# Kernel tuning notes

Hardware: AMD Instinct MI355X
Metric: run time of the kernel (lower is better)

The kernel has to match this reference:

```python
import jax, jax.numpy as jnp
import numpy as np

W_DIM = 512
FREQ = 1024
CH = 512
OUT_CH = 512
SIZE = 64
SR = 64.0
BW = 2.0
MAX_BW = BW * 8.0
B = 16
K = 3


def setup_inputs() -> dict:
    key = jax.random.key(0)
    ks = jax.random.split(key, 10)
    w = jax.random.normal(ks[0], (B, W_DIM), dtype=jnp.float32)
    # SynthesisInput buffers: random unit-direction freqs scaled by uniform radius in [0, max_bw)
    f = jax.random.normal(ks[1], (FREQ, 2), dtype=jnp.float32)
    f = f / jnp.linalg.norm(f, axis=1, keepdims=True)
    freqs = f * (jax.random.uniform(ks[2], (FREQ, 1), dtype=jnp.float32) * MAX_BW)
    phases = jax.random.uniform(ks[3], (FREQ,), dtype=jnp.float32) - 0.5
    input_weight = jax.random.normal(ks[4], (CH, FREQ), dtype=jnp.float32)
    # affine: FullyConnectedLayer(w_dim, 4, weight_init=0, bias_init=[1,0,0,0])
    affine_w = jnp.zeros((4, W_DIM), dtype=jnp.float32)
    affine_b = jnp.array([1.0, 0.0, 0.0, 0.0], dtype=jnp.float32)
    # per-layer style affine (w -> in_channels), bias_init=1 (StyleGAN convention)
    style_w = jax.random.normal(ks[5], (CH, W_DIM), dtype=jnp.float32)
    style_b = jnp.ones((CH,), dtype=jnp.float32)
    conv_w = jax.random.normal(ks[6], (OUT_CH, CH, K, K), dtype=jnp.float32)
    conv_b = jnp.zeros((OUT_CH,), dtype=jnp.float32)
    return {"w": w, "affine_w": affine_w, "affine_b": affine_b, "freqs": freqs,
            "phases": phases, "input_weight": input_weight, "style_w": style_w,
            "style_b": style_b, "conv_w": conv_w, "conv_b": conv_b}


def _fc(x, weight, bias):
    # FullyConnectedLayer: weight_gain = 1/sqrt(in_features)
    gain = 1.0 / np.sqrt(weight.shape[1])
    return x @ (weight * gain).T + bias


def _synthesis_input(w, affine_w, affine_b, freqs, phases, input_weight):
    t = _fc(w, affine_w, affine_b)                                  # [B,4]
    t = t / jnp.linalg.norm(t[:, :2], axis=1, keepdims=True)
    c, s, tx, ty = t[:, 0], t[:, 1], t[:, 2], t[:, 3]
    # m = m_r @ m_t (only the 2x3 top block matters)
    rot = jnp.stack([jnp.stack([c, -s], -1), jnp.stack([s, c], -1)], 1)  # [B,2,2]
    trans = jnp.stack([-tx, -ty], -1)                               # [B,2]
    shift = jnp.einsum('bij,bj->bi', rot, trans)                    # [B,2]
    phases_b = phases[None, :] + jnp.einsum('fi,bi->bf', freqs, shift)
    freqs_b = jnp.einsum('fi,bij->bfj', freqs, rot)                 # [B,F,2]
    amp = jnp.clip(1.0 - (jnp.linalg.norm(freqs_b, axis=2) - BW) / (SR / 2.0 - BW), 0.0, 1.0)
    # affine_grid(theta=diag(0.5*size/sr)=0.5, align_corners=False)
    theta00 = 0.5 * SIZE / SR
    xs = ((jnp.arange(SIZE, dtype=jnp.float32) + 0.5) / SIZE * 2.0 - 1.0) * theta00
    ys = ((jnp.arange(SIZE, dtype=jnp.float32) + 0.5) / SIZE * 2.0 - 1.0) * theta00
    gx, gy = jnp.meshgrid(xs, ys)                                   # [H,W]
    grid = jnp.stack([gx, gy], axis=-1)                             # [H,W,2]
    x = jnp.einsum('hwi,bfi->bhwf', grid, freqs_b) + phases_b[:, None, None, :]
    x = jnp.sin(x * (2.0 * np.pi)) * amp[:, None, None, :]
    effect_freq = jnp.sum((jnp.linalg.norm(freqs, axis=-1) < BW).astype(jnp.float32))
    x = jnp.einsum('bhwf,cf->bchw', x, input_weight / jnp.sqrt(effect_freq))
    return x                                                        # [B,CH,H,W]


def _modulated_conv2d(x, weight, s, padding=1):
    # demodulate: pre-normalize w and s
    w_hat = weight * jax.lax.rsqrt(jnp.mean(jnp.square(weight), axis=(1, 2, 3), keepdims=True))
    s_hat = s * jax.lax.rsqrt(jnp.mean(jnp.square(s)))
    # dcoefs[b,o] = rsqrt(sum_ikl (w[o,i,k,l]*s[b,i])^2 + eps)
    dcoefs = jax.lax.rsqrt(jnp.einsum('oikl,bi->bo', jnp.square(w_hat), jnp.square(s_hat)) + 1e-8)
    # grouped-per-sample conv == scale input channels by s, conv with base w, scale out by dcoefs
    x = x * s_hat[:, :, None, None]
    y = jax.lax.conv_general_dilated(x, w_hat, window_strides=(1, 1),
                                     padding=[(padding, padding), (padding, padding)],
                                     dimension_numbers=('NCHW', 'OIHW', 'NCHW'))
    return y * dcoefs[:, :, None, None]


def reference(w, affine_w, affine_b, freqs, phases, input_weight, style_w, style_b, conv_w, conv_b):
    x = _synthesis_input(w, affine_w, affine_b, freqs, phases, input_weight)
    s = _fc(w, style_w, style_b)                                    # [B,CH]
    y = _modulated_conv2d(x, conv_w, s, padding=K // 2)
    y = y + conv_b[None, :, None, None]
    y = jnp.where(y >= 0, y, 0.2 * y) * np.sqrt(2.0)                # lrelu + gain (bias_act)
    y = jnp.clip(y, -256.0, 256.0)                                  # conv_clamp
    return y
```

## Files before the change

### kernel.cpp

```cpp
#include <hip/hip_runtime.h>

typedef __attribute__((ext_vector_type(4))) float f32x4;
typedef __attribute__((ext_vector_type(8))) __bf16 bf16x8;

__device__ __forceinline__ unsigned short f2bf(float f) {
  unsigned int u = __builtin_bit_cast(unsigned int, f);
  return (unsigned short)((u + 0x7FFFu + ((u >> 16) & 1u)) >> 16);
}

__device__ __forceinline__ float sin2pi(float x) {
#if __has_builtin(__builtin_amdgcn_sinf) && __has_builtin(__builtin_amdgcn_fractf)
  return __builtin_amdgcn_sinf(__builtin_amdgcn_fractf(x));
#else
  return __sinf(x * 6.283185307179586f);
#endif
}

__device__ __forceinline__ void gll16(const void* g, void* l) {
  __builtin_amdgcn_global_load_lds(
      (const __attribute__((address_space(1))) void*)g,
      (__attribute__((address_space(3))) void*)l, 16, 0, 0);
}

template <int W>
__device__ __forceinline__ void vmwait() {
  if constexpr (W == 0) asm volatile("s_waitcnt vmcnt(0)" ::: "memory");
  else if constexpr (W == 2) asm volatile("s_waitcnt vmcnt(2)" ::: "memory");
  else if constexpr (W == 4) asm volatile("s_waitcnt vmcnt(4)" ::: "memory");
  else if constexpr (W == 6) asm volatile("s_waitcnt vmcnt(6)" ::: "memory");
  else if constexpr (W == 8) asm volatile("s_waitcnt vmcnt(8)" ::: "memory");
}

#define CFENCE() asm volatile("" ::: "memory")

__global__ void prep_freq_k(const float* __restrict__ w, const float* __restrict__ affine_w,
                            const float* __restrict__ affine_b, const float* __restrict__ freqs,
                            const float* __restrict__ phases, float4* __restrict__ freq_data,
                            float* __restrict__ scal) {
  const int b = blockIdx.x, tid = threadIdx.x;
  const int wv = tid >> 6, lane = tid & 63;
  __shared__ float tdot[4];
  __shared__ float par[4];
  __shared__ float scnt;
  float sum = 0.f;
  for (int i = lane; i < 512; i += 64) sum += w[b * 512 + i] * affine_w[wv * 512 + i];
#pragma unroll
  for (int o = 32; o > 0; o >>= 1) sum += __shfl_down(sum, o);
  if (lane == 0) tdot[wv] = sum;
  if (tid == 0) scnt = 0.f;
  __syncthreads();
  if (tid == 0) {
    const float gain = 0.04419417382415922f;
    float t0 = tdot[0] * gain + affine_b[0];
    float t1 = tdot[1] * gain + affine_b[1];
    float t2 = tdot[2] * gain + affine_b[2];
    float t3 = tdot[3] * gain + affine_b[3];
    float inv = 1.f / sqrtf(t0 * t0 + t1 * t1);
    float c = t0 * inv, s = t1 * inv, tx = t2 * inv, ty = t3 * inv;
    par[0] = c; par[1] = s;
    par[2] = -c * tx + s * ty;
    par[3] = -s * tx - c * ty;
  }
  __syncthreads();
  const float c = par[0], s = par[1], sh0 = par[2], sh1 = par[3];
  float cnt = 0.f;
  for (int f = tid; f < 1024; f += 256) {
    float fx = freqs[2 * f], fy = freqs[2 * f + 1];
    float fb0 = fx * c + fy * s;
    float fb1 = fy * c - fx * s;
    float ph = phases[f] + fx * sh0 + fy * sh1;
    float nb = sqrtf(fb0 * fb0 + fb1 * fb1);
    float amp = fminf(fmaxf(1.f - (nb - 2.f) * (1.f / 30.f), 0.f), 1.f);
    float4 v; v.x = fb0; v.y = fb1; v.z = ph; v.w = amp;
    freq_data[(b << 10) + f] = v;
    if (sqrtf(fx * fx + fy * fy) < 2.f) cnt += 1.f;
  }
  if (b == 0) {
    atomicAdd(&scnt, cnt);
    __syncthreads();
    if (tid == 0) scal[0] = 1.f / sqrtf(scnt);
  }
}

__global__ void style_k(const float* __restrict__ w, const float* __restrict__ style_w,
                        const float* __restrict__ style_b, float* __restrict__ s_out) {
  int idx = blockIdx.x * 256 + threadIdx.x;
  int b = idx >> 9, c = idx & 511;
  const float gain = 0.04419417382415922f;
  const float4* wr = (const float4*)(w + b * 512);
  const float4* sr = (const float4*)(style_w + (size_t)c * 512);
  float sum = 0.f;
#pragma unroll 4
  for (int i = 0; i < 128; ++i) {
    float4 a = wr[i], q = sr[i];
    sum += a.x * q.x + a.y * q.y + a.z * q.z + a.w * q.w;
  }
  s_out[idx] = sum * gain + style_b[c];
}

__global__ void convw_prep_k(const float* __restrict__ conv_w, float* __restrict__ wsumT,
                             unsigned short* __restrict__ bt_conv) {
  const int o = blockIdx.x, tid = threadIdx.x;
  __shared__ float red[256];
  float sum = 0.f;
  for (int i = tid; i < 4608; i += 256) { float v = conv_w[o * 4608 + i]; sum += v * v; }
  red[tid] = sum;
  __syncthreads();
  for (int off = 128; off > 0; off >>= 1) {
    if (tid < off) red[tid] += red[tid + off];
    __syncthreads();
  }
  const float rn = rsqrtf(red[0] * (1.f / 4608.f));
  for (int i = tid; i < 512; i += 256) {
    float sq = 0.f;
#pragma unroll
    for (int kl = 0; kl < 9; ++kl) {
      float v = conv_w[(o * 512 + i) * 9 + kl];
      sq += v * v;
      bt_conv[o * 4608 + kl * 512 + i] = f2bf(v * rn);
    }
    wsumT[i * 512 + o] = sq * rn * rn;
  }
}

__global__ void iw_cast_k(const float* __restrict__ iw, unsigned short* __restrict__ iw_bf) {
  int i = blockIdx.x * 256 + threadIdx.x;
  iw_bf[i] = f2bf(iw[i]);
}

__global__ void shat_dcoef_k(const float* __restrict__ s, const float* __restrict__ wsumT,
                             float* __restrict__ s_hat, float* __restrict__ dcoefs) {
  const int b = blockIdx.x, tid = threadIdx.x;
  __shared__ float red[256];
  __shared__ float sh2[512];
  float sum = 0.f;
  for (int i = tid; i < 8192; i += 256) { float v = s[i]; sum += v * v; }
  red[tid] = sum;
  __syncthreads();
  for (int off = 128; off > 0; off >>= 1) {
    if (tid < off) red[tid] += red[tid + off];
    __syncthreads();
  }
  const float inv_rms = rsqrtf(red[0] * (1.f / 8192.f));
  for (int c = tid; c < 512; c += 256) {
    float sh = s[b * 512 + c] * inv_rms;
    s_hat[b * 512 + c] = sh;
    sh2[c] = sh * sh;
  }
  __syncthreads();
  for (int o = tid; o < 512; o += 256) {
    float acc = 0.f;
    for (int i = 0; i < 512; ++i) acc += wsumT[i * 512 + o] * sh2[i];
    dcoefs[b * 512 + o] = rsqrtf(acc + 1e-8f);
  }
}

__global__ void border_zero_k(unsigned short* __restrict__ xmp) {
  int idx = blockIdx.x * 256 + threadIdx.x;
  int chunk = idx & 63;
  int t = idx >> 6;
  int p = t % 260;
  int b = t / 260;
  int h, w;
  if (p < 66) { h = 0; w = p; }
  else if (p < 132) { h = 65; w = p - 66; }
  else if (p < 196) { h = p - 131; w = 0; }
  else { h = p - 195; w = 65; }
  uint4 z; z.x = 0; z.y = 0; z.z = 0; z.w = 0;
  *(uint4*)&xmp[(((size_t)b * 66 + h) * 66 + w) * 512 + chunk * 8] = z;
}

__device__ __forceinline__ void sy_sgB(char* lB, const unsigned short* iw, int n0, int d,
                                       int rb, int kt, int lane, int lsw) {
  const unsigned short* src = iw + (size_t)(n0 + rb + (lane >> 3)) * 1024 + (kt << 6) + lsw;
  gll16(src, lB + d * 32768 + rb * 128);
}

__global__ __launch_bounds__(256, 2) void synth_gemm2_k(
    const float4* __restrict__ freq_data, const unsigned short* __restrict__ iw_bf,
    const float* __restrict__ s_hat, const float* __restrict__ scal,
    unsigned short* __restrict__ xmp) {
  extern __shared__ char sl[];
  char* lA = sl;
  char* lB = sl + 16384;
  const int bid = blockIdx.x;
  const int mt = bid >> 1, nt = bid & 1;
  const int m0 = mt << 7, n0 = nt << 8;
  const int b = m0 >> 12;
  const int hbase = (m0 >> 6) & 63;
  const int tid = threadIdx.x, lane = tid & 63, wv = tid >> 6;
  const int wm = (wv >> 1) << 6, wn = (wv & 1) << 7;
  const int g = tid & 15;
  const int r0 = (tid >> 4) << 3;
  const int lsw = (((lane & 7) ^ (lane >> 3)) << 3);
  const int aswz = (((lane >> 4) << 4)) ^ ((lane & 7) << 4);
  const char* pA = lA + (size_t)(wm + (lane & 15)) * 128;
  const int browB = wn + (lane & 15);
  f32x4 acc[4][8];
#pragma unroll
  for (int mi = 0; mi < 4; ++mi)
#pragma unroll
    for (int ni = 0; ni < 8; ++ni) { f32x4 z = {0.f, 0.f, 0.f, 0.f}; acc[mi][ni] = z; }
  const float gy0 = (hbase + 0.5f) * 0.015625f - 0.5f;
  const float gy1 = (hbase + 1.5f) * 0.015625f - 0.5f;

#pragma unroll
  for (int ig = 0; ig < 8; ++ig) sy_sgB(lB, iw_bf, n0, 0, wv * 64 + ig * 8, 0, lane, lsw);
  vmwait<0>();
  __builtin_amdgcn_s_barrier();
  CFENCE();

  for (int kt = 0; kt < 16; ++kt) {
    if (kt < 15) {
#pragma unroll
      for (int ig = 0; ig < 8; ++ig)
        sy_sgB(lB, iw_bf, n0, (kt + 1) & 1, wv * 64 + ig * 8, kt + 1, lane, lsw);
    }
    const float4* fdp = freq_data + (b << 10) + (kt << 6) + (g << 2);
    float4 fd0 = fdp[0], fd1 = fdp[1], fd2 = fdp[2], fd3 = fdp[3];
#pragma unroll
    for (int j = 0; j < 8; ++j) {
      const int r = r0 + j;
      const float gx = ((r & 63) + 0.5f) * 0.015625f - 0.5f;
      const float gy = (r >> 6) ? gy1 : gy0;
      ushort4 u;
      u.x = f2bf(sin2pi(gx * fd0.x + gy * fd0.y + fd0.z) * fd0.w);
      u.y = f2bf(sin2pi(gx * fd1.x + gy * fd1.y + fd1.z) * fd1.w);
      u.z = f2bf(sin2pi(gx * fd2.x + gy * fd2.y + fd2.z) * fd2.w);
      u.w = f2bf(sin2pi(gx * fd3.x + gy * fd3.y + fd3.z) * fd3.w);
      *(ushort4*)(lA + r * 128 + ((g << 3) ^ (j << 4))) = u;
    }
    asm volatile("s_waitcnt lgkmcnt(0)" ::: "memory");
    if (kt < 15) vmwait<8>(); else vmwait<0>();
    __builtin_amdgcn_s_barrier();
    CFENCE();
    __builtin_amdgcn_sched_barrier(0);

    const char* pB = lB + ((kt & 1) << 15) + (size_t)browB * 128;
#pragma unroll
    for (int ks = 0; ks < 2; ++ks) {
      const int ao = aswz ^ (ks << 6);
      bf16x8 af[4], bq[8];
#pragma unroll
      for (int mi = 0; mi < 4; ++mi) af[mi] = *(const bf16x8*)(pA + mi * 2048 + ao);
#pragma unroll
      for (int ni = 0; ni < 8; ++ni) bq[ni] = *(const bf16x8*)(pB + ni * 2048 + ao);
      __builtin_amdgcn_s_setprio(1);
#pragma unroll
      for (int mi = 0; mi < 4; ++mi)
#pragma unroll
        for (int ni = 0; ni < 8; ++ni)
          acc[mi][ni] = __builtin_amdgcn_mfma_f32_16x16x32_bf16(af[mi], bq[ni], acc[mi][ni], 0, 0, 0);
      __builtin_amdgcn_s_setprio(0);
    }
    CFENCE();
    __builtin_amdgcn_s_barrier();
    CFENCE();
  }

  const float inv_eff = scal[0];
  const int c_lo = lane & 15, r_hi = (lane >> 4) << 2;
#pragma unroll
  for (int ni = 0; ni < 8; ++ni) {
    const int cc = n0 + wn + (ni << 4) + c_lo;
    const float sc = s_hat[b * 512 + cc] * inv_eff;
#pragma unroll
    for (int mi = 0; mi < 4; ++mi) {
#pragma unroll
      for (int j = 0; j < 4; ++j) {
        const int rr = wm + (mi << 4) + r_hi + j;
        const int hp = hbase + (rr >> 6) + 1;
        const int wp = (rr & 63) + 1;
        xmp[(((size_t)b * 66 + hp) * 66 + wp) * 512 + cc] = f2bf(acc[mi][ni][j] * sc);
      }
    }
  }
}

__device__ __forceinline__ float epi_act(float a, float dco, float cb) {
  float y = a * dco + cb;
  y = (y >= 0.f ? y : 0.2f * y) * 1.4142135623730951f;
  return fminf(fmaxf(y, -256.f), 256.f);
}

struct ConvCtx {
  const unsigned short* xmp;
  const unsigned short* bt;
  int n0, hb, b_img, lane;
  int lsw;
  int gB_rb0;
  int gA_lo;
  int gA_up;
};

__device__ __forceinline__ void tile_geom(int t, int& dh, int& dw, int& kc, int& koff) {
  const int kc8 = t / 9;
  const int off = t - 9 * kc8;
  dh = off / 3;
  dw = off - 3 * dh;
  kc = kc8 << 6;
  koff = off * 512 + kc;
}

__device__ __forceinline__ void sgA(char* lds, const ConvCtx& c, int d, int rb,
                                    int dh, int dw, int kc) {
  const int r = rb + (c.lane >> 3);
  const int h = c.hb + (r >> 6) + dh;
  const int w = (r & 63) + dw;
  const unsigned short* src = c.xmp + (((size_t)c.b_img * 66 + h) * 66 + w) * 512 + kc + c.lsw;
  gll16(src, lds + d * 32768 + rb * 128);
}

__device__ __forceinline__ void sgB(char* lds, const ConvCtx& c, int d, int rb, int koff) {
  const int row = c.n0 + rb + (c.lane >> 3);
  const unsigned short* src = c.bt + (size_t)row * 4608 + koff + c.lsw;
  gll16(src, lds + 65536 + d * 32768 + rb * 128);
}

#define PHASE_SYNC()                                        \
  __builtin_amdgcn_s_barrier();                             \
  asm volatile("s_waitcnt lgkmcnt(0)" ::: "memory");        \
  __builtin_amdgcn_sched_barrier(0);

#define PHASE_END()                                         \
  CFENCE();                                                 \
  __builtin_amdgcn_s_barrier();                             \
  CFENCE();

template <int D, int W0, bool SB, bool SAU, bool SAL>
__device__ __forceinline__ void conv_tile(char* lds, const ConvCtx& c, f32x4 (&acc)[8][4],
                                          const char* pA, const char* pB, int aswz0, int t) {
  int dh1, dw1, kc1, koff1, dh2, dw2, kc2, koff2;
  tile_geom(t + 1, dh1, dw1, kc1, koff1);
  tile_geom(t + 2, dh2, dw2, kc2, koff2);
  const int a0 = aswz0, a1 = aswz0 ^ 64;
  bf16x8 bq[4];
  {
#pragma unroll
    for (int ni = 0; ni < 4; ++ni) bq[ni] = *(const bf16x8*)(pB + D * 32768 + ni * 2048 + a0);
    bf16x8 af[4];
#pragma unroll
    for (int i = 0; i < 4; ++i) af[i] = *(const bf16x8*)(pA + D * 32768 + i * 2048 + a0);
    if (SB) { sgB(lds, c, D ^ 1, c.gB_rb0, koff1); sgB(lds, c, D ^ 1, c.gB_rb0 + 8, koff1); }
    if (W0 >= 0) vmwait<W0>();
    PHASE_SYNC();
    __builtin_amdgcn_s_setprio(1);
#pragma unroll
    for (int i = 0; i < 4; ++i)
#pragma unroll
      for (int ni = 0; ni < 4; ++ni)
        acc[i][ni] = __builtin_amdgcn_mfma_f32_16x16x32_bf16(af[i], bq[ni], acc[i][ni], 0, 0, 0);
    __builtin_amdgcn_s_setprio(0);
    PHASE_END();
  }
  {
    bf16x8 af[4];
#pragma unroll
    for (int i = 0; i < 4; ++i) af[i] = *(const bf16x8*)(pA + D * 32768 + (4 + i) * 2048 + a0);
    if (SB) { sgB(lds, c, D ^ 1, c.gB_rb0 + 16, koff1); sgB(lds, c, D ^ 1, c.gB_rb0 + 24, koff1); }
    PHASE_SYNC();
    __builtin_amdgcn_s_setprio(1);
#pragma unroll
    for (int i = 0; i < 4; ++i)
#pragma unroll
      for (int ni = 0; ni < 4; ++ni)
        acc[4 + i][ni] = __builtin_amdgcn_mfma_f32_16x16x32_bf16(af[i], bq[ni], acc[4 + i][ni], 0, 0, 0);
    __builtin_amdgcn_s_setprio(0);
    PHASE_END();
  }
  {
#pragma unroll
    for (int ni = 0; ni < 4; ++ni) bq[ni] = *(const bf16x8*)(pB + D * 32768 + ni * 2048 + a1);
    bf16x8 af[4];
#pragma unroll
    for (int i = 0; i < 4; ++i) af[i] = *(const bf16x8*)(pA + D * 32768 + i * 2048 + a1);
    if (SAU) { sgA(lds, c, D ^ 1, c.gA_up, dh1, dw1, kc1); sgA(lds, c, D ^ 1, c.gA_up + 8, dh1, dw1, kc1); }
    PHASE_SYNC();
    __builtin_amdgcn_s_setprio(1);
#pragma unroll
    for (int i = 0; i < 4; ++i)
#pragma unroll
      for (int ni = 0; ni < 4; ++ni)
        acc[i][ni] = __builtin_amdgcn_mfma_f32_16x16x32_bf16(af[i], bq[ni], acc[i][ni], 0, 0, 0);
    __builtin_amdgcn_s_setprio(0);
    PHASE_END();
  }
  {
    bf16x8 af[4];
#pragma unroll
    for (int i = 0; i < 4; ++i) af[i] = *(const bf16x8*)(pA + D * 32768 + (4 + i) * 2048 + a1);
    if (SAL) { sgA(lds, c, D, c.gA_lo, dh2, dw2, kc2); sgA(lds, c, D, c.gA_lo + 8, dh2, dw2, kc2); }
    PHASE_SYNC();
    __builtin_amdgcn_s_setprio(1);
#pragma unroll
    for (int i = 0; i < 4; ++i)
#pragma unroll
      for (int ni = 0; ni < 4; ++ni)
        acc[4 + i][ni] = __builtin_amdgcn_mfma_f32_16x16x32_bf16(af[i], bq[ni], acc[4 + i][ni], 0, 0, 0);
    __builtin_amdgcn_s_setprio(0);
    PHASE_END();
  }
}

__global__ __launch_bounds__(512, 2) void conv_gemm8_k(
    const unsigned short* __restrict__ xmp, const unsigned short* __restrict__ bt_conv,
    const float* __restrict__ dcoefs, const float* __restrict__ conv_b,
    float* __restrict__ out) {
  extern __shared__ char lds[];
  const int tid = threadIdx.x, lane = tid & 63, wv = tid >> 6;
  const int bid = blockIdx.x;
  const int wg = (bid & 7) * 64 + (bid >> 3);
  const int mt = wg >> 1, nt = wg & 1;
  const int m0 = mt << 8, n0 = nt << 8;
  const int b_img = m0 >> 12;
  const int hb = (m0 >> 6) & 63;
  const int wm = (wv >> 2) << 7, wn = (wv & 3) << 6;

  ConvCtx c;
  c.xmp = xmp; c.bt = bt_conv;
  c.n0 = n0; c.hb = hb; c.b_img = b_img; c.lane = lane;
  c.lsw = (((lane & 7) ^ (lane >> 3)) << 3);
  c.gB_rb0 = (((wv & 3) >> 1) << 7) + (((wv & 1) | ((wv >> 2) << 1)) << 5);
  c.gA_lo = wm + ((wv & 3) << 4);
  c.gA_up = c.gA_lo + 64;

  const char* pA = lds + (size_t)(wm + (lane & 15)) * 128;
  const char* pB = lds + 65536 + (size_t)(wn + (lane & 15)) * 128;
  const int aswz0 = (((lane >> 4) << 4)) ^ ((lane & 7) << 4);

  f32x4 acc[8][4];
#pragma unroll
  for (int mi = 0; mi < 8; ++mi)
#pragma unroll
    for (int ni = 0; ni < 4; ++ni) { f32x4 z = {0.f, 0.f, 0.f, 0.f}; acc[mi][ni] = z; }

  sgB(lds, c, 0, c.gB_rb0, 0);       sgB(lds, c, 0, c.gB_rb0 + 8, 0);
  sgB(lds, c, 0, c.gB_rb0 + 16, 0);  sgB(lds, c, 0, c.gB_rb0 + 24, 0);
  sgA(lds, c, 0, c.gA_up, 0, 0, 0);  sgA(lds, c, 0, c.gA_up + 8, 0, 0, 0);
  sgA(lds, c, 0, c.gA_lo, 0, 0, 0);  sgA(lds, c, 0, c.gA_lo + 8, 0, 0, 0);
  {
    int dh1, dw1, kc1, koff1;
    tile_geom(1, dh1, dw1, kc1, koff1);
    sgA(lds, c, 1, c.gA_lo, dh1, dw1, kc1);
    sgA(lds, c, 1, c.gA_lo + 8, dh1, dw1, kc1);
  }
  vmwait<2>();
  __builtin_amdgcn_s_barrier();
  CFENCE();

  for (int it = 0; it < 35; ++it) {
    conv_tile<0, 4, true, true, true>(lds, c, acc, pA, pB, aswz0, 2 * it);
    conv_tile<1, 4, true, true, true>(lds, c, acc, pA, pB, aswz0, 2 * it + 1);
  }
  conv_tile<0, 4, true, true, false>(lds, c, acc, pA, pB, aswz0, 70);
  conv_tile<1, 0, false, false, false>(lds, c, acc, pA, pB, aswz0, 71);

  const int c_lo = lane & 15, r_hi = (lane >> 4) << 2;
#pragma unroll
  for (int ni = 0; ni < 4; ++ni) {
    const int oo = n0 + wn + (ni << 4) + c_lo;
    const float dco = dcoefs[b_img * 512 + oo];
    const float cb = conv_b[oo];
#pragma unroll
    for (int mi = 0; mi < 8; ++mi) {
      const int rr = wm + (mi << 4) + r_hi;
      const int hh = hb + (rr >> 6);
      const int w0 = rr & 63;
      float4 v;
      v.x = epi_act(acc[mi][ni][0], dco, cb);
      v.y = epi_act(acc[mi][ni][1], dco, cb);
      v.z = epi_act(acc[mi][ni][2], dco, cb);
      v.w = epi_act(acc[mi][ni][3], dco, cb);
      *(float4*)&out[(((size_t)b_img * 512 + oo) * 64 + hh) * 64 + w0] = v;
    }
  }
}

extern "C" void kernel_launch(void* const* d_in, const int* in_sizes, int n_in,
                              void* d_out, int out_size, void* d_ws, size_t ws_size,
                              hipStream_t stream) {
  (void)in_sizes; (void)n_in; (void)out_size;
  const float* w        = (const float*)d_in[0];
  const float* affine_w = (const float*)d_in[1];
  const float* affine_b = (const float*)d_in[2];
  const float* freqs    = (const float*)d_in[3];
  const float* phases   = (const float*)d_in[4];
  const float* input_weight = (const float*)d_in[5];
  const float* style_w  = (const float*)d_in[6];
  const float* style_b  = (const float*)d_in[7];
  const float* conv_w   = (const float*)d_in[8];
  const float* conv_b   = (const float*)d_in[9];
  float* out = (float*)d_out;

  char* p = (char*)d_ws;
  float4* freq_data = (float4*)p;               p += (size_t)16 * 1024 * 16;
  float* scal = (float*)p;                      p += 256;
  float* s_buf = (float*)p;                     p += 8192 * 4;
  float* s_hat = (float*)p;                     p += 8192 * 4;
  float* wsumT = (float*)p;                     p += (size_t)512 * 512 * 4;
  float* dcoefs = (float*)p;                    p += 8192 * 4;
  unsigned short* iw_bf = (unsigned short*)p;   p += (size_t)512 * 1024 * 2;
  unsigned short* bt_conv = (unsigned short*)p; p += (size_t)512 * 4608 * 2;
  unsigned short* xmp = (unsigned short*)p;     p += (size_t)16 * 66 * 66 * 512 * 2;
  if (ws_size < (size_t)(p - (char*)d_ws)) return;

  (void)hipFuncSetAttribute((const void*)conv_gemm8_k,
                            hipFuncAttributeMaxDynamicSharedMemorySize, 131072);
  (void)hipFuncSetAttribute((const void*)synth_gemm2_k,
                            hipFuncAttributeMaxDynamicSharedMemorySize, 81920);

  border_zero_k<<<1040, 256, 0, stream>>>(xmp);
  prep_freq_k<<<16, 256, 0, stream>>>(w, affine_w, affine_b, freqs, phases, freq_data, scal);
  style_k<<<32, 256, 0, stream>>>(w, style_w, style_b, s_buf);
  convw_prep_k<<<512, 256, 0, stream>>>(conv_w, wsumT, bt_conv);
  iw_cast_k<<<2048, 256, 0, stream>>>(input_weight, iw_bf);
  shat_dcoef_k<<<16, 256, 0, stream>>>(s_buf, wsumT, s_hat, dcoefs);
  synth_gemm2_k<<<1024, 256, 81920, stream>>>(freq_data, iw_bf, s_hat, scal, xmp);
  conv_gemm8_k<<<512, 512, 131072, stream>>>(xmp, bt_conv, dcoefs, conv_b, out);
}
```

Measured before the change: 425.4 us.

## Simplify conv GEMM main loop to one barrier per K-tile double buffer

```diff
diff --git a/kernel.cpp b/kernel.cpp
--- a/kernel.cpp
+++ b/kernel.cpp
@@ -317,89 +317,70 @@
   gll16(src, lds + 65536 + d * 32768 + rb * 128);
 }
 
-#define PHASE_SYNC()                                        \
-  __builtin_amdgcn_s_barrier();                             \
-  asm volatile("s_waitcnt lgkmcnt(0)" ::: "memory");        \
+template <bool STG>
+__device__ __forceinline__ void conv_tile1(char* lds, const ConvCtx& c, f32x4 (&acc)[8][4],
+                                           const char* pA, const char* pB, int aswz0, int t) {
+  int dh1, dw1, kc1, koff1;
+  tile_geom(t + 1, dh1, dw1, kc1, koff1);
+  const int D = t & 1, Dn = D ^ 1;
+  const int db = D << 15;
+  const int a0 = aswz0, a1 = aswz0 ^ 64;
+
+  vmwait<0>();
+  __builtin_amdgcn_s_barrier();
+  CFENCE();
   __builtin_amdgcn_sched_barrier(0);
 
-#define PHASE_END()                                         \
-  CFENCE();                                                 \
-  __builtin_amdgcn_s_barrier();                             \
+  bf16x8 bq[4], af[4];
+#pragma unroll
+  for (int ni = 0; ni < 4; ++ni) bq[ni] = *(const bf16x8*)(pB + db + ni * 2048 + a0);
+#pragma unroll
+  for (int i = 0; i < 4; ++i) af[i] = *(const bf16x8*)(pA + db + i * 2048 + a0);
+  if (STG) {
+    sgB(lds, c, Dn, c.gB_rb0, koff1);      sgB(lds, c, Dn, c.gB_rb0 + 8, koff1);
+    sgB(lds, c, Dn, c.gB_rb0 + 16, koff1); sgB(lds, c, Dn, c.gB_rb0 + 24, koff1);
+  }
+  __builtin_amdgcn_s_setprio(1);
+#pragma unroll
+  for (int i = 0; i < 4; ++i)
+#pragma unroll
+    for (int ni = 0; ni < 4; ++ni)
+      acc[i][ni] = __builtin_amdgcn_mfma_f32_16x16x32_bf16(af[i], bq[ni], acc[i][ni], 0, 0, 0);
+  __builtin_amdgcn_s_setprio(0);
+#pragma unroll
+  for (int i = 0; i < 4; ++i) af[i] = *(const bf16x8*)(pA + db + (4 + i) * 2048 + a0);
+  if (STG) {
+    sgA(lds, c, Dn, c.gA_up, dh1, dw1, kc1); sgA(lds, c, Dn, c.gA_up + 8, dh1, dw1, kc1);
+    sgA(lds, c, Dn, c.gA_lo, dh1, dw1, kc1); sgA(lds, c, Dn, c.gA_lo + 8, dh1, dw1, kc1);
+  }
+  __builtin_amdgcn_s_setprio(1);
+#pragma unroll
+  for (int i = 0; i < 4; ++i)
+#pragma unroll
+    for (int ni = 0; ni < 4; ++ni)
+      acc[4 + i][ni] = __builtin_amdgcn_mfma_f32_16x16x32_bf16(af[i], bq[ni], acc[4 + i][ni], 0, 0, 0);
+  __builtin_amdgcn_s_setprio(0);
+#pragma unroll
+  for (int ni = 0; ni < 4; ++ni) bq[ni] = *(const bf16x8*)(pB + db + ni * 2048 + a1);
+#pragma unroll
+  for (int i = 0; i < 4; ++i) af[i] = *(const bf16x8*)(pA + db + i * 2048 + a1);
+  __builtin_amdgcn_s_setprio(1);
+#pragma unroll
+  for (int i = 0; i < 4; ++i)
+#pragma unroll
+    for (int ni = 0; ni < 4; ++ni)
+      acc[i][ni] = __builtin_amdgcn_mfma_f32_16x16x32_bf16(af[i], bq[ni], acc[i][ni], 0, 0, 0);
+  __builtin_amdgcn_s_setprio(0);
+#pragma unroll
+  for (int i = 0; i < 4; ++i) af[i] = *(const bf16x8*)(pA + db + (4 + i) * 2048 + a1);
+  __builtin_amdgcn_s_setprio(1);
+#pragma unroll
+  for (int i = 0; i < 4; ++i)
+#pragma unroll
+    for (int ni = 0; ni < 4; ++ni)
+      acc[4 + i][ni] = __builtin_amdgcn_mfma_f32_16x16x32_bf16(af[i], bq[ni], acc[4 + i][ni], 0, 0, 0);
+  __builtin_amdgcn_s_setprio(0);
   CFENCE();
-
-template <int D, int W0, bool SB, bool SAU, bool SAL>
-__device__ __forceinline__ void conv_tile(char* lds, const ConvCtx& c, f32x4 (&acc)[8][4],
-                                          const char* pA, const char* pB, int aswz0, int t) {
-  int dh1, dw1, kc1, koff1, dh2, dw2, kc2, koff2;
-  tile_geom(t + 1, dh1, dw1, kc1, koff1);
-  tile_geom(t + 2, dh2, dw2, kc2, koff2);
-  const int a0 = aswz0, a1 = aswz0 ^ 64;
-  bf16x8 bq[4];
-  {
-#pragma unroll
-    for (int ni = 0; ni < 4; ++ni) bq[ni] = *(const bf16x8*)(pB + D * 32768 + ni * 2048 + a0);
-    bf16x8 af[4];
-#pragma unroll
-    for (int i = 0; i < 4; ++i) af[i] = *(const bf16x8*)(pA + D * 32768 + i * 2048 + a0);
-    if (SB) { sgB(lds, c, D ^ 1, c.gB_rb0, koff1); sgB(lds, c, D ^ 1, c.gB_rb0 + 8, koff1); }
-    if (W0 >= 0) vmwait<W0>();
-    PHASE_SYNC();
-    __builtin_amdgcn_s_setprio(1);
-#pragma unroll
-    for (int i = 0; i < 4; ++i)
-#pragma unroll
-      for (int ni = 0; ni < 4; ++ni)
-        acc[i][ni] = __builtin_amdgcn_mfma_f32_16x16x32_bf16(af[i], bq[ni], acc[i][ni], 0, 0, 0);
-    __builtin_amdgcn_s_setprio(0);
-    PHASE_END();
-  }
-  {
-    bf16x8 af[4];
-#pragma unroll
-    for (int i = 0; i < 4; ++i) af[i] = *(const bf16x8*)(pA + D * 32768 + (4 + i) * 2048 + a0);
-    if (SB) { sgB(lds, c, D ^ 1, c.gB_rb0 + 16, koff1); sgB(lds, c, D ^ 1, c.gB_rb0 + 24, koff1); }
-    PHASE_SYNC();
-    __builtin_amdgcn_s_setprio(1);
-#pragma unroll
-    for (int i = 0; i < 4; ++i)
-#pragma unroll
-      for (int ni = 0; ni < 4; ++ni)
-        acc[4 + i][ni] = __builtin_amdgcn_mfma_f32_16x16x32_bf16(af[i], bq[ni], acc[4 + i][ni], 0, 0, 0);
-    __builtin_amdgcn_s_setprio(0);
-    PHASE_END();
-  }
-  {
-#pragma unroll
-    for (int ni = 0; ni < 4; ++ni) bq[ni] = *(const bf16x8*)(pB + D * 32768 + ni * 2048 + a1);
-    bf16x8 af[4];
-#pragma unroll
-    for (int i = 0; i < 4; ++i) af[i] = *(const bf16x8*)(pA + D * 32768 + i * 2048 + a1);
-    if (SAU) { sgA(lds, c, D ^ 1, c.gA_up, dh1, dw1, kc1); sgA(lds, c, D ^ 1, c.gA_up + 8, dh1, dw1, kc1); }
-    PHASE_SYNC();
-    __builtin_amdgcn_s_setprio(1);
-#pragma unroll
-    for (int i = 0; i < 4; ++i)
-#pragma unroll
-      for (int ni = 0; ni < 4; ++ni)
-        acc[i][ni] = __builtin_amdgcn_mfma_f32_16x16x32_bf16(af[i], bq[ni], acc[i][ni], 0, 0, 0);
-    __builtin_amdgcn_s_setprio(0);
-    PHASE_END();
-  }
-  {
-    bf16x8 af[4];
-#pragma unroll
-    for (int i = 0; i < 4; ++i) af[i] = *(const bf16x8*)(pA + D * 32768 + (4 + i) * 2048 + a1);
-    if (SAL) { sgA(lds, c, D, c.gA_lo, dh2, dw2, kc2); sgA(lds, c, D, c.gA_lo + 8, dh2, dw2, kc2); }
-    PHASE_SYNC();
-    __builtin_amdgcn_s_setprio(1);
-#pragma unroll
-    for (int i = 0; i < 4; ++i)
-#pragma unroll
-      for (int ni = 0; ni < 4; ++ni)
-        acc[4 + i][ni] = __builtin_amdgcn_mfma_f32_16x16x32_bf16(af[i], bq[ni], acc[4 + i][ni], 0, 0, 0);
-    __builtin_amdgcn_s_setprio(0);
-    PHASE_END();
-  }
 }
 
 __global__ __launch_bounds__(512, 2) void conv_gemm8_k(
@@ -438,22 +419,9 @@
   sgB(lds, c, 0, c.gB_rb0 + 16, 0);  sgB(lds, c, 0, c.gB_rb0 + 24, 0);
   sgA(lds, c, 0, c.gA_up, 0, 0, 0);  sgA(lds, c, 0, c.gA_up + 8, 0, 0, 0);
   sgA(lds, c, 0, c.gA_lo, 0, 0, 0);  sgA(lds, c, 0, c.gA_lo + 8, 0, 0, 0);
-  {
-    int dh1, dw1, kc1, koff1;
-    tile_geom(1, dh1, dw1, kc1, koff1);
-    sgA(lds, c, 1, c.gA_lo, dh1, dw1, kc1);
-    sgA(lds, c, 1, c.gA_lo + 8, dh1, dw1, kc1);
-  }
-  vmwait<2>();
-  __builtin_amdgcn_s_barrier();
-  CFENCE();
-
-  for (int it = 0; it < 35; ++it) {
-    conv_tile<0, 4, true, true, true>(lds, c, acc, pA, pB, aswz0, 2 * it);
-    conv_tile<1, 4, true, true, true>(lds, c, acc, pA, pB, aswz0, 2 * it + 1);
-  }
-  conv_tile<0, 4, true, true, false>(lds, c, acc, pA, pB, aswz0, 70);
-  conv_tile<1, 0, false, false, false>(lds, c, acc, pA, pB, aswz0, 71);
+
+  for (int t = 0; t < 71; ++t) conv_tile1<true>(lds, c, acc, pA, pB, aswz0, t);
+  conv_tile1<false>(lds, c, acc, pA, pB, aswz0, 71);
 
   const int c_lo = lane & 15, r_hi = (lane >> 4) << 2;
 #pragma unroll
```

Measured after the change: 418.1 us. Within noise of the previous version (-1.7%).
